# Performance work log

Hardware: AMD Instinct MI355X
Metric: run time of the kernel (lower is better)

## Reference

```python
import jax, jax.numpy as jnp
import numpy as np

B, N = 32, 14            # hardcoded in the torch module
IN_F, OUT_F, H = 1024, 1024, 4
ALPHA = 0.2              # leaky relu negative slope
NEG = -9e15


def setup_inputs() -> dict:
    key = jax.random.key(0)
    ks = jax.random.split(key, 6)
    # xavier-uniform-ish scales (exact init values don't affect correctness testing)
    x = jax.random.normal(ks[0], (B, N, IN_F), dtype=jnp.float32)
    adj = jax.random.normal(ks[1], (B, N, N), dtype=jnp.float32)
    W = jax.random.normal(ks[2], (H, B, IN_F, OUT_F), dtype=jnp.float32) * (1.414 / np.sqrt(IN_F))
    a = jax.random.normal(ks[3], (H, B, 2 * OUT_F, 1), dtype=jnp.float32) * (1.414 / np.sqrt(2 * OUT_F))
    fc_w = jax.random.normal(ks[4], (H, OUT_F, N * OUT_F), dtype=jnp.float32) * (1.0 / np.sqrt(N * OUT_F))
    fc_b = jnp.zeros((H, OUT_F), dtype=jnp.float32)
    return {"x": x, "adj": adj, "W": W, "a": a, "fc_w": fc_w, "fc_b": fc_b}


def reference(x, adj, W, a, fc_w, fc_b):
    # Wh: [H, B, N, OUT_F]
    Wh = jnp.einsum('bni,hbio->hbno', x, W)
    a1 = a[:, :, :OUT_F, 0]   # [H, B, OUT_F]
    a2 = a[:, :, OUT_F:, 0]   # [H, B, OUT_F]
    Wh1 = jnp.einsum('hbno,hbo->hbn', Wh, a1)  # [H, B, N]
    Wh2 = jnp.einsum('hbno,hbo->hbn', Wh, a2)  # [H, B, N]
    e = jax.nn.leaky_relu(Wh1[..., :, None] + Wh2[..., None, :], negative_slope=ALPHA)  # [H,B,N,N]
    att = jnp.where(adj[None] > 0, e, NEG)
    # torch F.softmax(attention, dim=1) on [B,N,N] -> axis=2 here (first node axis)
    att = jax.nn.softmax(att, axis=2)
    # dropout p=0 (eval) -> no-op
    h_prime = jnp.einsum('hbnm,hbmo->hbno', att, Wh).reshape(H, B, N * OUT_F)
    out_h = jnp.einsum('hbf,hof->hbo', h_prime, fc_w) + fc_b[:, None, :]  # [H, B, OUT_F]
    out = out_h.sum(axis=0)                                              # [B, OUT_F]
    return jax.nn.log_softmax(out, axis=1)
```

## Files before the change

### kernel.cpp

```cpp
#include <hip/hip_runtime.h>
#include <hip/hip_bf16.h>

#define ALPHA 0.2f
#define NEGV  -9000000000000000.0f

typedef __attribute__((ext_vector_type(8))) short bf16x8;
typedef __attribute__((ext_vector_type(4))) float f32x4;

__device__ __forceinline__ short f2b(float f) {
  unsigned u = __float_as_uint(f);
  unsigned r = (u + 0x7FFFu + ((u >> 16) & 1u)) >> 16;
  return (short)r;
}

__global__ __launch_bounds__(256) void k1_wh(const float* __restrict__ x,
                                             const float* __restrict__ W,
                                             float* __restrict__ Whp) {
  int blk = blockIdx.x;
  int kc = blk & 3;
  int hb = blk >> 2;
  int b  = hb & 31;
  int t  = threadIdx.x;
  __shared__ float xs[14][256];
  int i0 = kc * 256;
  const float* xb = x + (size_t)b * 14 * 1024 + i0;
  #pragma unroll
  for (int n = 0; n < 14; ++n) xs[n][t] = xb[n * 1024 + t];
  __syncthreads();

  const float* Wp = W + ((size_t)hb * 1024 + i0) * 1024 + 4 * t;
  float4 acc[14];
  #pragma unroll
  for (int n = 0; n < 14; ++n) acc[n] = make_float4(0.f, 0.f, 0.f, 0.f);

  for (int ii = 0; ii < 256; ii += 4) {
    float4 w0 = *(const float4*)(Wp + (size_t)(ii + 0) * 1024);
    float4 w1 = *(const float4*)(Wp + (size_t)(ii + 1) * 1024);
    float4 w2 = *(const float4*)(Wp + (size_t)(ii + 2) * 1024);
    float4 w3 = *(const float4*)(Wp + (size_t)(ii + 3) * 1024);
    #pragma unroll
    for (int n = 0; n < 14; ++n) {
      float4 xn = *(const float4*)&xs[n][ii];
      acc[n].x += xn.x * w0.x + xn.y * w1.x + xn.z * w2.x + xn.w * w3.x;
      acc[n].y += xn.x * w0.y + xn.y * w1.y + xn.z * w2.y + xn.w * w3.y;
      acc[n].z += xn.x * w0.z + xn.y * w1.z + xn.z * w2.z + xn.w * w3.z;
      acc[n].w += xn.x * w0.w + xn.y * w1.w + xn.z * w2.w + xn.w * w3.w;
    }
  }

  float* dst = Whp + (size_t)kc * 1835008 + (size_t)hb * 14336 + 4 * t;
  #pragma unroll
  for (int n = 0; n < 14; ++n) *(float4*)(dst + n * 1024) = acc[n];
}

__global__ __launch_bounds__(256) void k1b_red(const float* __restrict__ p,
                                               float* __restrict__ Wh) {
  size_t idx = ((size_t)blockIdx.x * 256 + threadIdx.x) * 4;
  const size_t S = 1835008;
  float4 a = *(const float4*)(p + idx);
  float4 b = *(const float4*)(p + S + idx);
  float4 c = *(const float4*)(p + 2 * S + idx);
  float4 d = *(const float4*)(p + 3 * S + idx);
  a.x += b.x + c.x + d.x;
  a.y += b.y + c.y + d.y;
  a.z += b.z + c.z + d.z;
  a.w += b.w + c.w + d.w;
  *(float4*)(Wh + idx) = a;
}

__global__ __launch_bounds__(128) void k2_att(const float* __restrict__ Wh,
                                              const float* __restrict__ adj,
                                              const float* __restrict__ a,
                                              float* __restrict__ att) {
  int hb = blockIdx.x;
  int b  = hb & 31;
  int t  = threadIdx.x;
  int l  = t & 63, w = t >> 6;
  __shared__ float wh1s[14], wh2s[14];
  const float* whp = Wh + (size_t)hb * 14336;
  const float* a1  = a + (size_t)hb * 2048;
  const float* a2  = a1 + 1024;

  for (int nn = 0; nn < 7; ++nn) {
    int n = w * 7 + nn;
    float p1 = 0.f, p2 = 0.f;
    #pragma unroll
    for (int j = 0; j < 16; ++j) {
      int o = l + 64 * j;
      float wv = whp[n * 1024 + o];
      p1 += wv * a1[o];
      p2 += wv * a2[o];
    }
    #pragma unroll
    for (int s = 32; s >= 1; s >>= 1) {
      p1 += __shfl_xor(p1, s);
      p2 += __shfl_xor(p2, s);
    }
    if (l == 0) { wh1s[n] = p1; wh2s[n] = p2; }
  }
  __syncthreads();

  if (t < 14) {
    int m = t;
    const float* adjb = adj + b * 196;
    float col[14];
    float mx = -1e30f;
    #pragma unroll
    for (int n = 0; n < 14; ++n) {
      float e = wh1s[n] + wh2s[m];
      e = (e > 0.f) ? e : ALPHA * e;
      e = (adjb[n * 14 + m] > 0.f) ? e : NEGV;
      col[n] = e;
      mx = fmaxf(mx, e);
    }
    float s = 0.f;
    #pragma unroll
    for (int n = 0; n < 14; ++n) { col[n] = expf(col[n] - mx); s += col[n]; }
    float inv = 1.f / s;
    #pragma unroll
    for (int n = 0; n < 14; ++n) att[hb * 196 + n * 14 + m] = col[n] * inv;
  }
}

__global__ __launch_bounds__(128) void k3_hprime(const float* __restrict__ Wh,
                                                 const float* __restrict__ att,
                                                 float* __restrict__ hp) {
  int blk = blockIdx.x;
  int hb = blk >> 1, oc = blk & 1;
  int t = threadIdx.x;
  __shared__ float att_s[196];
  for (int idx = t; idx < 196; idx += 128) att_s[idx] = att[hb * 196 + idx];
  __syncthreads();

  int o4 = oc * 512 + 4 * t;
  const float* whp = Wh + (size_t)hb * 14336;
  float4 acc[14];
  #pragma unroll
  for (int n = 0; n < 14; ++n) acc[n] = make_float4(0.f, 0.f, 0.f, 0.f);
  #pragma unroll
  for (int m = 0; m < 14; ++m) {
    float4 wm = *(const float4*)(whp + m * 1024 + o4);
    #pragma unroll
    for (int n = 0; n < 14; ++n) {
      float anm = att_s[n * 14 + m];
      acc[n].x += anm * wm.x;
      acc[n].y += anm * wm.y;
      acc[n].z += anm * wm.z;
      acc[n].w += anm * wm.w;
    }
  }
  float* dst = hp + (size_t)hb * 14336 + o4;
  #pragma unroll
  for (int n = 0; n < 14; ++n) *(float4*)(dst + n * 1024) = acc[n];
}

__global__ __launch_bounds__(256) void k4_fc(const float* __restrict__ hp,
                                             const float* __restrict__ fcw,
                                             float* __restrict__ oaccp) {
  int blk = blockIdx.x;
  int kc = blk & 7;
  int oc = (blk >> 3) & 15;
  int h  = blk >> 7;
  int t = threadIdx.x;
  int lane = t & 63, w = t >> 6;
  int mw = w & 1, nw = w >> 1;
  __shared__ __align__(16) short As[32][272];
  __shared__ __align__(16) short Bs[64][272];
  const int o0 = oc * 64;
  const size_t hpb = (size_t)h * 32 * 14336;
  const size_t fwb = (size_t)h * 1024 * 14336;
  f32x4 c0 = {0.f, 0.f, 0.f, 0.f};
  f32x4 c1 = {0.f, 0.f, 0.f, 0.f};

  for (int tt = 0; tt < 7; ++tt) {
    int f0 = kc * 1792 + tt * 256;
    #pragma unroll
    for (int p = 0; p < 8; ++p) {
      int f4 = p * 256 + t;
      int row = f4 >> 6, c4 = f4 & 63;
      float4 wv = *(const float4*)(hp + hpb + (size_t)row * 14336 + f0 + 4 * c4);
      short4 s4 = make_short4(f2b(wv.x), f2b(wv.y), f2b(wv.z), f2b(wv.w));
      *(short4*)&As[row][4 * c4] = s4;
    }
    #pragma unroll
    for (int p = 0; p < 16; ++p) {
      int f4 = p * 256 + t;
      int row = f4 >> 6, c4 = f4 & 63;
      float4 wv = *(const float4*)(fcw + fwb + (size_t)(o0 + row) * 14336 + f0 + 4 * c4);
      short4 s4 = make_short4(f2b(wv.x), f2b(wv.y), f2b(wv.z), f2b(wv.w));
      *(short4*)&Bs[row][4 * c4] = s4;
    }
    __syncthreads();
    #pragma unroll
    for (int ks = 0; ks < 8; ++ks) {
      bf16x8 af = *(const bf16x8*)&As[mw * 16 + (lane & 15)][ks * 32 + (lane >> 4) * 8];
      bf16x8 b0 = *(const bf16x8*)&Bs[nw * 32 + (lane & 15)][ks * 32 + (lane >> 4) * 8];
      bf16x8 b1 = *(const bf16x8*)&Bs[nw * 32 + 16 + (lane & 15)][ks * 32 + (lane >> 4) * 8];
      c0 = __builtin_amdgcn_mfma_f32_16x16x32_bf16(af, b0, c0, 0, 0, 0);
      c1 = __builtin_amdgcn_mfma_f32_16x16x32_bf16(af, b1, c1, 0, 0, 0);
    }
    __syncthreads();
  }
  float* op = oaccp + (size_t)(kc * 4 + h) * 32768;
  int br   = mw * 16 + (lane >> 4) * 4;
  int ocol = o0 + nw * 32 + (lane & 15);
  #pragma unroll
  for (int r = 0; r < 4; ++r) {
    op[(br + r) * 1024 + ocol]      = c0[r];
    op[(br + r) * 1024 + ocol + 16] = c1[r];
  }
}

__global__ __launch_bounds__(256) void k5_lsm(const float* __restrict__ oaccp,
                                              const float* __restrict__ fcb,
                                              float* __restrict__ out) {
  int b = blockIdx.x, t = threadIdx.x;
  int lane = t & 63, wid = t >> 6;
  __shared__ float redm[4], reds[4];
  float v[4];
  float mx = -1e30f;
  #pragma unroll
  for (int j = 0; j < 4; ++j) {
    int o = t + 256 * j;
    float val = fcb[o] + fcb[1024 + o] + fcb[2048 + o] + fcb[3072 + o];
    #pragma unroll
    for (int p = 0; p < 32; ++p) val += oaccp[(size_t)p * 32768 + b * 1024 + o];
    v[j] = val;
    mx = fmaxf(mx, val);
  }
  #pragma unroll
  for (int s = 32; s >= 1; s >>= 1) mx = fmaxf(mx, __shfl_xor(mx, s));
  if (lane == 0) redm[wid] = mx;
  __syncthreads();
  mx = fmaxf(fmaxf(redm[0], redm[1]), fmaxf(redm[2], redm[3]));
  float sm = 0.f;
  #pragma unroll
  for (int j = 0; j < 4; ++j) sm += expf(v[j] - mx);
  #pragma unroll
  for (int s = 32; s >= 1; s >>= 1) sm += __shfl_xor(sm, s);
  if (lane == 0) reds[wid] = sm;
  __syncthreads();
  sm = reds[0] + reds[1] + reds[2] + reds[3];
  float lse = mx + logf(sm);
  #pragma unroll
  for (int j = 0; j < 4; ++j) {
    int o = t + 256 * j;
    out[b * 1024 + o] = v[j] - lse;
  }
}

extern "C" void kernel_launch(void* const* d_in, const int* in_sizes, int n_in,
                              void* d_out, int out_size, void* d_ws, size_t ws_size,
                              hipStream_t stream) {
  const float* x   = (const float*)d_in[0];
  const float* adj = (const float*)d_in[1];
  const float* W   = (const float*)d_in[2];
  const float* a   = (const float*)d_in[3];
  const float* fcw = (const float*)d_in[4];
  const float* fcb = (const float*)d_in[5];
  float* out = (float*)d_out;

  char* ws = (char*)d_ws;
  float* Whp = (float*)(ws);
  float* Wh  = (float*)(ws + 29360128);
  float* att = (float*)(ws + 36700160);
  float* hp  = (float*)(ws + 36800512);
  float* oap = (float*)(ws + 44140544);

  k1_wh<<<512, 256, 0, stream>>>(x, W, Whp);
  k1b_red<<<1792, 256, 0, stream>>>(Whp, Wh);
  k2_att<<<128, 128, 0, stream>>>(Wh, adj, a, att);
  k3_hprime<<<256, 128, 0, stream>>>(Wh, att, hp);
  k4_fc<<<512, 256, 0, stream>>>(hp, fcw, oap);
  k5_lsm<<<32, 256, 0, stream>>>(oap, fcb, out);
}
```

Measured before the change: 897.1 us.

## Fuse Wh partial reduction and attention scores into neighboring kernels

Computes the a1/a2 dot products directly from the k1 accumulators as per-split partials. It then removes the separate reduction and attention kernels: the new k3 sums the four split-K partials of Wh on the fly and computes the softmax in shared memory. Also adds register double-buffering of W loads in k1 and vectorizes k5 loads and stores. This cuts two launches and the Wh/att round trips through global memory, at the cost of k3 reading four partial buffers and some extra shuffles in k1.

```diff
diff --git a/kernel.cpp b/kernel.cpp
--- a/kernel.cpp
+++ b/kernel.cpp
@@ -15,15 +15,18 @@
 
 __global__ __launch_bounds__(256) void k1_wh(const float* __restrict__ x,
                                              const float* __restrict__ W,
-                                             float* __restrict__ Whp) {
+                                             const float* __restrict__ a,
+                                             float* __restrict__ Whp,
+                                             float* __restrict__ dp) {
   int blk = blockIdx.x;
   int kc = blk & 3;
   int hb = blk >> 2;
   int b  = hb & 31;
   int t  = threadIdx.x;
   __shared__ float xs[14][256];
+  __shared__ float red[4][28];
   int i0 = kc * 256;
-  const float* xb = x + (size_t)b * 14 * 1024 + i0;
+  const float* xb = x + (size_t)b * 14336 + i0;
   #pragma unroll
   for (int n = 0; n < 14; ++n) xs[n][t] = xb[n * 1024 + t];
   __syncthreads();
@@ -33,11 +36,16 @@
   #pragma unroll
   for (int n = 0; n < 14; ++n) acc[n] = make_float4(0.f, 0.f, 0.f, 0.f);
 
-  for (int ii = 0; ii < 256; ii += 4) {
-    float4 w0 = *(const float4*)(Wp + (size_t)(ii + 0) * 1024);
-    float4 w1 = *(const float4*)(Wp + (size_t)(ii + 1) * 1024);
-    float4 w2 = *(const float4*)(Wp + (size_t)(ii + 2) * 1024);
-    float4 w3 = *(const float4*)(Wp + (size_t)(ii + 3) * 1024);
+  float4 w0 = *(const float4*)(Wp);
+  float4 w1 = *(const float4*)(Wp + 1024);
+  float4 w2 = *(const float4*)(Wp + 2048);
+  float4 w3 = *(const float4*)(Wp + 3072);
+  for (int ii = 0; ii < 256; ii += 8) {
+    int j1 = (ii + 4) & 255;
+    float4 n0 = *(const float4*)(Wp + (size_t)(j1    ) * 1024);
+    float4 n1 = *(const float4*)(Wp + (size_t)(j1 + 1) * 1024);
+    float4 n2 = *(const float4*)(Wp + (size_t)(j1 + 2) * 1024);
+    float4 n3 = *(const float4*)(Wp + (size_t)(j1 + 3) * 1024);
     #pragma unroll
     for (int n = 0; n < 14; ++n) {
       float4 xn = *(const float4*)&xs[n][ii];
@@ -46,60 +54,62 @@
       acc[n].z += xn.x * w0.z + xn.y * w1.z + xn.z * w2.z + xn.w * w3.z;
       acc[n].w += xn.x * w0.w + xn.y * w1.w + xn.z * w2.w + xn.w * w3.w;
     }
+    int j2 = (ii + 8) & 255;
+    w0 = *(const float4*)(Wp + (size_t)(j2    ) * 1024);
+    w1 = *(const float4*)(Wp + (size_t)(j2 + 1) * 1024);
+    w2 = *(const float4*)(Wp + (size_t)(j2 + 2) * 1024);
+    w3 = *(const float4*)(Wp + (size_t)(j2 + 3) * 1024);
+    #pragma unroll
+    for (int n = 0; n < 14; ++n) {
+      float4 xn = *(const float4*)&xs[n][ii + 4];
+      acc[n].x += xn.x * n0.x + xn.y * n1.x + xn.z * n2.x + xn.w * n3.x;
+      acc[n].y += xn.x * n0.y + xn.y * n1.y + xn.z * n2.y + xn.w * n3.y;
+      acc[n].z += xn.x * n0.z + xn.y * n1.z + xn.z * n2.z + xn.w * n3.z;
+      acc[n].w += xn.x * n0.w + xn.y * n1.w + xn.z * n2.w + xn.w * n3.w;
+    }
   }
 
   float* dst = Whp + (size_t)kc * 1835008 + (size_t)hb * 14336 + 4 * t;
   #pragma unroll
   for (int n = 0; n < 14; ++n) *(float4*)(dst + n * 1024) = acc[n];
-}
-
-__global__ __launch_bounds__(256) void k1b_red(const float* __restrict__ p,
-                                               float* __restrict__ Wh) {
-  size_t idx = ((size_t)blockIdx.x * 256 + threadIdx.x) * 4;
-  const size_t S = 1835008;
-  float4 a = *(const float4*)(p + idx);
-  float4 b = *(const float4*)(p + S + idx);
-  float4 c = *(const float4*)(p + 2 * S + idx);
-  float4 d = *(const float4*)(p + 3 * S + idx);
-  a.x += b.x + c.x + d.x;
-  a.y += b.y + c.y + d.y;
-  a.z += b.z + c.z + d.z;
-  a.w += b.w + c.w + d.w;
-  *(float4*)(Wh + idx) = a;
-}
-
-__global__ __launch_bounds__(128) void k2_att(const float* __restrict__ Wh,
-                                              const float* __restrict__ adj,
-                                              const float* __restrict__ a,
-                                              float* __restrict__ att) {
-  int hb = blockIdx.x;
-  int b  = hb & 31;
-  int t  = threadIdx.x;
-  int l  = t & 63, w = t >> 6;
-  __shared__ float wh1s[14], wh2s[14];
-  const float* whp = Wh + (size_t)hb * 14336;
-  const float* a1  = a + (size_t)hb * 2048;
-  const float* a2  = a1 + 1024;
-
-  for (int nn = 0; nn < 7; ++nn) {
-    int n = w * 7 + nn;
-    float p1 = 0.f, p2 = 0.f;
-    #pragma unroll
-    for (int j = 0; j < 16; ++j) {
-      int o = l + 64 * j;
-      float wv = whp[n * 1024 + o];
-      p1 += wv * a1[o];
-      p2 += wv * a2[o];
-    }
+
+  const float* ap = a + (size_t)hb * 2048 + 4 * t;
+  float4 a1v = *(const float4*)ap;
+  float4 a2v = *(const float4*)(ap + 1024);
+  int lane = t & 63, w = t >> 6;
+  #pragma unroll
+  for (int n = 0; n < 14; ++n) {
+    float p1 = acc[n].x * a1v.x + acc[n].y * a1v.y + acc[n].z * a1v.z + acc[n].w * a1v.w;
+    float p2 = acc[n].x * a2v.x + acc[n].y * a2v.y + acc[n].z * a2v.z + acc[n].w * a2v.w;
     #pragma unroll
     for (int s = 32; s >= 1; s >>= 1) {
       p1 += __shfl_xor(p1, s);
       p2 += __shfl_xor(p2, s);
     }
-    if (l == 0) { wh1s[n] = p1; wh2s[n] = p2; }
-  }
-  __syncthreads();
-
+    if (lane == 0) { red[w][n] = p1; red[w][14 + n] = p2; }
+  }
+  __syncthreads();
+  if (t < 28) {
+    dp[((size_t)kc * 128 + hb) * 28 + t] =
+        red[0][t] + red[1][t] + red[2][t] + red[3][t];
+  }
+}
+
+__global__ __launch_bounds__(128) void k3_atthp(const float* __restrict__ Whp,
+                                                const float* __restrict__ dp,
+                                                const float* __restrict__ adj,
+                                                float* __restrict__ hp) {
+  int blk = blockIdx.x;
+  int hb = blk >> 1, oc = blk & 1;
+  int b  = hb & 31;
+  int t  = threadIdx.x;
+  __shared__ float wh1s[14], wh2s[14], att_s[196];
+  if (t < 28) {
+    const float* d = dp + (size_t)hb * 28 + t;
+    float v = d[0] + d[3584] + d[7168] + d[10752];
+    if (t < 14) wh1s[t] = v; else wh2s[t - 14] = v;
+  }
+  __syncthreads();
   if (t < 14) {
     int m = t;
     const float* adjb = adj + b * 196;
@@ -118,28 +128,27 @@
     for (int n = 0; n < 14; ++n) { col[n] = expf(col[n] - mx); s += col[n]; }
     float inv = 1.f / s;
     #pragma unroll
-    for (int n = 0; n < 14; ++n) att[hb * 196 + n * 14 + m] = col[n] * inv;
-  }
-}
-
-__global__ __launch_bounds__(128) void k3_hprime(const float* __restrict__ Wh,
-                                                 const float* __restrict__ att,
-                                                 float* __restrict__ hp) {
-  int blk = blockIdx.x;
-  int hb = blk >> 1, oc = blk & 1;
-  int t = threadIdx.x;
-  __shared__ float att_s[196];
-  for (int idx = t; idx < 196; idx += 128) att_s[idx] = att[hb * 196 + idx];
+    for (int n = 0; n < 14; ++n) att_s[n * 14 + m] = col[n] * inv;
+  }
   __syncthreads();
 
   int o4 = oc * 512 + 4 * t;
-  const float* whp = Wh + (size_t)hb * 14336;
+  const float* wp0 = Whp + (size_t)hb * 14336 + o4;
+  const size_t S = 1835008;
   float4 acc[14];
   #pragma unroll
   for (int n = 0; n < 14; ++n) acc[n] = make_float4(0.f, 0.f, 0.f, 0.f);
   #pragma unroll
   for (int m = 0; m < 14; ++m) {
-    float4 wm = *(const float4*)(whp + m * 1024 + o4);
+    const float* q = wp0 + (size_t)m * 1024;
+    float4 v0 = *(const float4*)(q);
+    float4 v1 = *(const float4*)(q + S);
+    float4 v2 = *(const float4*)(q + 2 * S);
+    float4 v3 = *(const float4*)(q + 3 * S);
+    float4 wm = make_float4(v0.x + v1.x + v2.x + v3.x,
+                            v0.y + v1.y + v2.y + v3.y,
+                            v0.z + v1.z + v2.z + v3.z,
+                            v0.w + v1.w + v2.w + v3.w);
     #pragma unroll
     for (int n = 0; n < 14; ++n) {
       float anm = att_s[n * 14 + m];
@@ -149,9 +158,9 @@
       acc[n].w += anm * wm.w;
     }
   }
-  float* dst = hp + (size_t)hb * 14336 + o4;
-  #pragma unroll
-  for (int n = 0; n < 14; ++n) *(float4*)(dst + n * 1024) = acc[n];
+  float* dsto = hp + (size_t)hb * 14336 + o4;
+  #pragma unroll
+  for (int n = 0; n < 14; ++n) *(float4*)(dsto + n * 1024) = acc[n];
 }
 
 __global__ __launch_bounds__(256) void k4_fc(const float* __restrict__ hp,
@@ -217,36 +226,34 @@
   int b = blockIdx.x, t = threadIdx.x;
   int lane = t & 63, wid = t >> 6;
   __shared__ float redm[4], reds[4];
-  float v[4];
-  float mx = -1e30f;
-  #pragma unroll
-  for (int j = 0; j < 4; ++j) {
-    int o = t + 256 * j;
-    float val = fcb[o] + fcb[1024 + o] + fcb[2048 + o] + fcb[3072 + o];
-    #pragma unroll
-    for (int p = 0; p < 32; ++p) val += oaccp[(size_t)p * 32768 + b * 1024 + o];
-    v[j] = val;
-    mx = fmaxf(mx, val);
-  }
+  float4 f0 = *(const float4*)(fcb + 4 * t);
+  float4 f1 = *(const float4*)(fcb + 1024 + 4 * t);
+  float4 f2 = *(const float4*)(fcb + 2048 + 4 * t);
+  float4 f3 = *(const float4*)(fcb + 3072 + 4 * t);
+  float4 v = make_float4(f0.x + f1.x + f2.x + f3.x,
+                         f0.y + f1.y + f2.y + f3.y,
+                         f0.z + f1.z + f2.z + f3.z,
+                         f0.w + f1.w + f2.w + f3.w);
+  #pragma unroll
+  for (int p = 0; p < 32; ++p) {
+    float4 o = *(const float4*)(oaccp + (size_t)p * 32768 + b * 1024 + 4 * t);
+    v.x += o.x; v.y += o.y; v.z += o.z; v.w += o.w;
+  }
+  float mx = fmaxf(fmaxf(v.x, v.y), fmaxf(v.z, v.w));
   #pragma unroll
   for (int s = 32; s >= 1; s >>= 1) mx = fmaxf(mx, __shfl_xor(mx, s));
   if (lane == 0) redm[wid] = mx;
   __syncthreads();
   mx = fmaxf(fmaxf(redm[0], redm[1]), fmaxf(redm[2], redm[3]));
-  float sm = 0.f;
-  #pragma unroll
-  for (int j = 0; j < 4; ++j) sm += expf(v[j] - mx);
+  float sm = expf(v.x - mx) + expf(v.y - mx) + expf(v.z - mx) + expf(v.w - mx);
   #pragma unroll
   for (int s = 32; s >= 1; s >>= 1) sm += __shfl_xor(sm, s);
   if (lane == 0) reds[wid] = sm;
   __syncthreads();
   sm = reds[0] + reds[1] + reds[2] + reds[3];
   float lse = mx + logf(sm);
-  #pragma unroll
-  for (int j = 0; j < 4; ++j) {
-    int o = t + 256 * j;
-    out[b * 1024 + o] = v[j] - lse;
-  }
+  float4 r = make_float4(v.x - lse, v.y - lse, v.z - lse, v.w - lse);
+  *(float4*)(out + b * 1024 + 4 * t) = r;
 }
 
 extern "C" void kernel_launch(void* const* d_in, const int* in_sizes, int n_in,
@@ -262,15 +269,12 @@
 
   char* ws = (char*)d_ws;
   float* Whp = (float*)(ws);
-  float* Wh  = (float*)(ws + 29360128);
-  float* att = (float*)(ws + 36700160);
-  float* hp  = (float*)(ws + 36800512);
-  float* oap = (float*)(ws + 44140544);
-
-  k1_wh<<<512, 256, 0, stream>>>(x, W, Whp);
-  k1b_red<<<1792, 256, 0, stream>>>(Whp, Wh);
-  k2_att<<<128, 128, 0, stream>>>(Wh, adj, a, att);
-  k3_hprime<<<256, 128, 0, stream>>>(Wh, att, hp);
+  float* dp  = (float*)(ws + 29360128);
+  float* hp  = (float*)(ws + 29417472);
+  float* oap = (float*)(ws + 36757504);
+
+  k1_wh<<<512, 256, 0, stream>>>(x, W, a, Whp, dp);
+  k3_atthp<<<256, 128, 0, stream>>>(Whp, dp, adj, hp);
   k4_fc<<<512, 256, 0, stream>>>(hp, fcw, oap);
   k5_lsm<<<32, 256, 0, stream>>>(oap, fcb, out);
 }
```

Measured after the change: 885.9 us. No clear change (-1.2%).
